# Optimization experiments

Measured on AMD Instinct MI355X. Metric: run time of the kernel, lower is better.

Reference implementation:

```python
import jax, jax.numpy as jnp
import numpy as np

N, E, B = 16000, 256000, 64
H = 4
DIMS = [960, 512, 256, 128]  # per-layer input dims; output dim of layer i is DIMS[i+1] = HID[i]*H
HID = [128, 64, 32]


def setup_inputs() -> dict:
    key = jax.random.key(0)
    ks = jax.random.split(key, 16)
    inp = {}
    inp["x"] = jax.random.normal(ks[0], (N, DIMS[0]), jnp.float32)
    inp["edge_index"] = jax.random.randint(ks[1], (2, E), 0, N)
    inp["batch"] = jnp.sort(jax.random.randint(ks[2], (N,), 0, B))
    k = 3
    for i in range(3):
        din, c = DIMS[i], HID[i]
        s = 1.0 / np.sqrt(din).astype(np.float32)
        inp[f"Wl{i+1}"] = jax.random.normal(ks[k], (din, H * c), jnp.float32) * s; k += 1
        inp[f"Wr{i+1}"] = jax.random.normal(ks[k], (din, H * c), jnp.float32) * s; k += 1
        inp[f"att{i+1}"] = jax.random.normal(ks[k], (H, c), jnp.float32) * (1.0 / np.sqrt(c).astype(np.float32)); k += 1
        inp[f"b{i+1}"] = jnp.zeros((H * c,), jnp.float32)
        inp[f"gnw{i+1}"] = jnp.ones((H * c,), jnp.float32)
        inp[f"gnb{i+1}"] = jnp.zeros((H * c,), jnp.float32)
        inp[f"gnm{i+1}"] = jnp.ones((H * c,), jnp.float32)
    d = DIMS[-1]
    inp["aW1"] = jax.random.normal(ks[k], (d, 128), jnp.float32) * (1.0 / np.sqrt(d).astype(np.float32)); k += 1
    inp["ab1"] = jnp.zeros((128,), jnp.float32)
    inp["aW2"] = jax.random.normal(ks[k], (128, 1), jnp.float32) * (1.0 / np.sqrt(128).astype(np.float32)); k += 1
    inp["ab2"] = jnp.zeros((1,), jnp.float32)
    return inp


def _gatv2(x, src, dst, Wl, Wr, att, bias):
    # PyG GATv2Conv, concat=True, negative_slope=0.2 (self-loops already in src/dst)
    n = x.shape[0]
    h, c = att.shape
    xl = (x @ Wl).reshape(n, h, c)
    xr = (x @ Wr).reshape(n, h, c)
    e = jax.nn.leaky_relu(xl[src] + xr[dst], negative_slope=0.2)  # [E,H,C]
    logit = jnp.einsum('ehc,hc->eh', e, att)                      # [E,H]
    m = jax.ops.segment_max(logit, dst, num_segments=n)
    m = jnp.nan_to_num(m, neginf=0.0)
    p = jnp.exp(logit - m[dst])
    z = jax.ops.segment_sum(p, dst, num_segments=n)
    alpha = p / (z[dst] + 1e-16)                                  # segment softmax over dst
    out = jax.ops.segment_sum(alpha[:, :, None] * xl[src], dst, num_segments=n)
    return out.reshape(n, h * c) + bias


def _graphnorm(x, w, b, ms, eps=1e-5):
    # PyG GraphNorm with batch=None: normalize over all nodes as one graph
    mean = jnp.mean(x, axis=0, keepdims=True)
    xc = x - ms * mean
    var = jnp.mean(xc * xc, axis=0, keepdims=True)
    return w * xc / jnp.sqrt(var + eps) + b


def reference(x, edge_index, batch,
              Wl1, Wr1, att1, b1, gnw1, gnb1, gnm1,
              Wl2, Wr2, att2, b2, gnw2, gnb2, gnm2,
              Wl3, Wr3, att3, b3, gnw3, gnb3, gnm3,
              aW1, ab1, aW2, ab2):
    n = x.shape[0]
    loop = jnp.arange(n)
    src = jnp.concatenate([edge_index[0], loop])  # add self-loops (PyG default)
    dst = jnp.concatenate([edge_index[1], loop])
    layers = [(Wl1, Wr1, att1, b1, gnw1, gnb1, gnm1),
              (Wl2, Wr2, att2, b2, gnw2, gnb2, gnm2),
              (Wl3, Wr3, att3, b3, gnw3, gnb3, gnm3)]
    for Wl, Wr, att, bb, gw, gb, gm in layers:
        x = _gatv2(x, src, dst, Wl, Wr, att, bb)
        x = _graphnorm(x, gw, gb, gm)
        x = jax.nn.relu(x)
    # AttentionalAggregation pooling: gate MLP -> segment softmax over graphs -> weighted sum
    gate = jax.nn.relu(x @ aW1 + ab1) @ aW2 + ab2  # [N,1]
    mg = jax.ops.segment_max(gate, batch, num_segments=B)
    mg = jnp.nan_to_num(mg, neginf=0.0)
    pg = jnp.exp(gate - mg[batch])
    zg = jax.ops.segment_sum(pg, batch, num_segments=B)
    a = pg / (zg[batch] + 1e-16)
    return jax.ops.segment_sum(a * x, batch, num_segments=B)  # [B, 128]
```

## Files before the change

### kernel.cpp

```cpp
#include <hip/hip_runtime.h>
#include <cstdint>
#include <cstddef>
#include <math.h>


typedef _Float16  h16x8  __attribute__((ext_vector_type(8)));
typedef _Float16  h16x4  __attribute__((ext_vector_type(4)));
typedef _Float16  h16x2  __attribute__((ext_vector_type(2)));
typedef float     f32x4  __attribute__((ext_vector_type(4)));

template<int R> struct HV;
template<> struct HV<8> { using T = h16x8; };
template<> struct HV<4> { using T = h16x4; };
template<> struct HV<2> { using T = h16x2; };

__device__ __forceinline__ void gload_lds16(const void* g, void* l) {
    __builtin_amdgcn_global_load_lds(
        (const __attribute__((address_space(1))) uint32_t*)g,
        (__attribute__((address_space(3))) uint32_t*)l, 16, 0, 0);
}

__device__ __forceinline__ int swz_k(int k, int row) {
    return (k & ~31) | ((((k >> 3) & 3) ^ ((row >> 1) & 3)) << 3) | (k & 7);
}

__device__ __forceinline__ void gn_coef(float s1, float s2, float w, float b,
                                        float ms, float invN, float& al, float& be) {
    float mean = s1 * invN;
    float ex2  = s2 * invN;
    float a    = ms * mean;
    float var  = ex2 - 2.f * a * mean + a * a;
    al = w * rsqrtf(var + 1e-5f);
    be = b - a * al;
}

__device__ __forceinline__ void conv_elem(int t, const float* __restrict__ Wl,
                                          const float* __restrict__ Wr,
                                          _Float16* __restrict__ Wt, int K, int HC) {
    int k = t / HC, n = t - k * HC;
    const int ks = swz_k(k, n);
    Wt[(size_t)n * K + ks] = (_Float16)Wl[t];
    if (Wr) Wt[(size_t)(HC + n) * K + ks] = (_Float16)Wr[t];
}

__global__ __launch_bounds__(256) void conv_all(
        const float* __restrict__ Wl0, const float* __restrict__ Wr0, _Float16* __restrict__ T0,
        const float* __restrict__ Wl1, const float* __restrict__ Wr1, _Float16* __restrict__ T1,
        const float* __restrict__ Wl2, const float* __restrict__ Wr2, _Float16* __restrict__ T2,
        const float* __restrict__ Wa, _Float16* __restrict__ Ta) {
    int t = blockIdx.x * blockDim.x + threadIdx.x;
    if (t < 491520) { conv_elem(t, Wl0, Wr0, T0, 960, 512); return; }
    t -= 491520;
    if (t < 131072) { conv_elem(t, Wl1, Wr1, T1, 512, 256); return; }
    t -= 131072;
    if (t < 32768)  { conv_elem(t, Wl2, Wr2, T2, 256, 128); return; }
    t -= 32768;
    if (t < 16384)  conv_elem(t, Wa, nullptr, Ta, 128, 128);
}

template<typename InT, bool NORM>
__global__ __launch_bounds__(256) void prep_a(
        const InT* __restrict__ X,
        const float* __restrict__ s1, const float* __restrict__ s2,
        const float* __restrict__ gw, const float* __restrict__ gb,
        const float* __restrict__ gm, float invN,
        _Float16* __restrict__ Out, int M, int K) {
    int t = blockIdx.x * blockDim.x + threadIdx.x;
    const int gpr = K >> 3;
    if (t >= M * gpr) return;
    int m = t / gpr, g = t - m * gpr;
    int k = g << 3;
    float uu[8];
    if constexpr (sizeof(InT) == 4) {
        const float* src = (const float*)X + (size_t)m * K + k;
        float4 u0 = *(const float4*)src;
        float4 u1 = *(const float4*)(src + 4);
        uu[0] = u0.x; uu[1] = u0.y; uu[2] = u0.z; uu[3] = u0.w;
        uu[4] = u1.x; uu[5] = u1.y; uu[6] = u1.z; uu[7] = u1.w;
    } else {
        h16x8 hv = *(const h16x8*)((const _Float16*)X + (size_t)m * K + k);
        #pragma unroll
        for (int j = 0; j < 8; ++j) uu[j] = (float)hv[j];
    }
    if (NORM) {
        #pragma unroll
        for (int j = 0; j < 8; ++j) {
            float al, be;
            gn_coef(s1[k + j], s2[k + j], gw[k + j], gb[k + j], gm[k + j],
                    invN, al, be);
            uu[j] = fmaxf(al * uu[j] + be, 0.f);
        }
    }
    h16x8 h;
    #pragma unroll
    for (int j = 0; j < 8; ++j) h[j] = (_Float16)uu[j];
    *(h16x8*)&Out[(size_t)m * K + swz_k(k, m)] = h;
}

template<bool BIAS, bool RELU, bool GATE, typename OutT>
__global__ __launch_bounds__(256) void mfma_gemm(
        const _Float16* __restrict__ A, const _Float16* __restrict__ Bt,
        const float* __restrict__ bias, OutT* __restrict__ C,
        OutT* __restrict__ C2, int CN,
        int M, int K, int N,
        const float* __restrict__ gw2, const float* __restrict__ gb2,
        float* __restrict__ gate) {
    __shared__ __attribute__((aligned(16))) _Float16 sA[2][128 * 32];
    __shared__ __attribute__((aligned(16))) _Float16 sB[2][128 * 32];
    __shared__ float gsum[128];

    const int gx  = gridDim.x;
    const int nwg = gx * gridDim.y;
    const int id  = blockIdx.y * gx + blockIdx.x;
    const int q   = nwg >> 3, r = nwg & 7;
    const int xcd = id & 7, sub = id >> 3;
    const int nid = (xcd < r) ? (xcd * (q + 1) + sub)
                              : (r * (q + 1) + (xcd - r) * q + sub);
    const int row0 = (nid / gx) * 128;
    const int col0 = (nid % gx) * 128;

    const int tid  = threadIdx.x;
    const int lane = tid & 63;
    const int w    = tid >> 6;
    const int wm   = w >> 1, wn = w & 1;
    const int lr   = lane & 15, lg = lane >> 4;
    const int bRow = w * 16 + (lane >> 2);
    const int bGrp = (lane & 3) * 8;
    const int fGrp = (lg ^ ((lr >> 1) & 3)) * 8;

    f32x4 acc[4][4] = {};

    const _Float16* pa = A  + (size_t)(row0 + bRow) * K + bGrp;
    const _Float16* pb = Bt + (size_t)(col0 + bRow) * K + bGrp;

    auto stage = [&](int buf, int k0) {
        gload_lds16(pa + k0,                  (char*)&sA[buf][0] + w * 1024);
        gload_lds16(pa + (size_t)64 * K + k0, (char*)&sA[buf][0] + 4096 + w * 1024);
        gload_lds16(pb + k0,                  (char*)&sB[buf][0] + w * 1024);
        gload_lds16(pb + (size_t)64 * K + k0, (char*)&sB[buf][0] + 4096 + w * 1024);
    };

    stage(0, 0);
    if (GATE) { if (tid < 128) gsum[tid] = 0.f; }
    __syncthreads();
    int cur = 0;
    for (int k0 = 0; k0 < K; k0 += 32) {
        if (k0 + 32 < K) stage(cur ^ 1, k0 + 32);
        h16x8 ah[4], bh[4];
        #pragma unroll
        for (int i = 0; i < 4; ++i) {
            ah[i] = *(const h16x8*)&sA[cur][(wm * 64 + i * 16 + lr) * 32 + fGrp];
            bh[i] = *(const h16x8*)&sB[cur][(wn * 64 + i * 16 + lr) * 32 + fGrp];
        }
        #pragma unroll
        for (int i = 0; i < 4; ++i)
            #pragma unroll
            for (int j = 0; j < 4; ++j)
                acc[i][j] = __builtin_amdgcn_mfma_f32_16x16x32_f16(ah[i], bh[j], acc[i][j], 0, 0, 0);
        __syncthreads();
        cur ^= 1;
    }

    if constexpr (!GATE) {
        OutT* co = (col0 < CN) ? C : C2;
        const int cb = (col0 < CN) ? col0 : col0 - CN;
        #pragma unroll
        for (int i = 0; i < 4; ++i) {
            const int rowb = row0 + wm * 64 + i * 16 + lg * 4;
            #pragma unroll
            for (int j = 0; j < 4; ++j) {
                const int col  = col0 + wn * 64 + j * 16 + lr;
                const int colw = cb   + wn * 64 + j * 16 + lr;
                const float bv = BIAS ? bias[col] : 0.f;
                #pragma unroll
                for (int qq = 0; qq < 4; ++qq) {
                    float v = acc[i][j][qq] + bv;
                    if (RELU) v = fmaxf(v, 0.f);
                    co[(size_t)(rowb + qq) * CN + colw] = (OutT)v;
                }
            }
        }
    } else {
        float gp[4][4] = {};
        float w2[4];
        #pragma unroll
        for (int j = 0; j < 4; ++j) w2[j] = gw2[wn * 64 + j * 16 + lr];
        #pragma unroll
        for (int i = 0; i < 4; ++i)
            #pragma unroll
            for (int j = 0; j < 4; ++j) {
                const int col = wn * 64 + j * 16 + lr;
                const float bv = bias[col];
                #pragma unroll
                for (int qq = 0; qq < 4; ++qq) {
                    float v = fmaxf(acc[i][j][qq] + bv, 0.f);
                    gp[i][qq] += v * w2[j];
                }
            }
        #pragma unroll
        for (int i = 0; i < 4; ++i)
            #pragma unroll
            for (int qq = 0; qq < 4; ++qq) {
                float pv = gp[i][qq];
                pv += __shfl_xor(pv, 1);
                pv += __shfl_xor(pv, 2);
                pv += __shfl_xor(pv, 4);
                pv += __shfl_xor(pv, 8);
                if (lr == 0) atomicAdd(&gsum[wm * 64 + i * 16 + lg * 4 + qq], pv);
            }
        __syncthreads();
        if (tid < 128) gate[row0 + tid] = gsum[tid] + gb2[0];
    }
}

__global__ void csr_count(const int* __restrict__ edst, int E, int Etot,
                          int* __restrict__ deg) {
    int e = blockIdx.x * blockDim.x + threadIdx.x;
    if (e >= Etot) return;
    int d = (e < E) ? edst[e] : e - E;
    atomicAdd(&deg[d], 1);
}

__global__ __launch_bounds__(1024) void scan_deg(const int* __restrict__ deg,
                                                 int* __restrict__ row_start,
                                                 int* __restrict__ cursor, int N) {
    __shared__ int part[1024];
    const int tid = threadIdx.x;
    const int base = tid * 16;
    int loc[16];
    int s = 0;
    #pragma unroll
    for (int j = 0; j < 16; ++j) {
        int i = base + j;
        s += (i < N) ? deg[i] : 0;
        loc[j] = s;
    }
    part[tid] = s; __syncthreads();
    #pragma unroll
    for (int off = 1; off < 1024; off <<= 1) {
        int t2 = (tid >= off) ? part[tid - off] : 0;
        __syncthreads();
        part[tid] += t2;
        __syncthreads();
    }
    const int pre = tid ? part[tid - 1] : 0;
    #pragma unroll
    for (int j = 0; j < 16; ++j) {
        int i = base + j;
        if (i < N) {
            int st = pre + (j ? loc[j - 1] : 0);
            row_start[i] = st;
            cursor[i]    = st;
            if (i == N - 1) row_start[N] = pre + loc[j];
        }
    }
}

__global__ void csr_fill(const int* __restrict__ esrc, const int* __restrict__ edst,
                         int E, int Etot, int* __restrict__ cursor,
                         int* __restrict__ src_perm) {
    int e = blockIdx.x * blockDim.x + threadIdx.x;
    if (e >= Etot) return;
    int s, d;
    if (e < E) { s = esrc[e]; d = edst[e]; }
    else       { s = d = e - E; }
    int pos = atomicAdd(&cursor[d], 1);
    src_perm[pos] = s;
}

template<int LOG2C>
__global__ __launch_bounds__(256) void gat_agg(
        const _Float16* __restrict__ xl, const _Float16* __restrict__ xr,
        const float* __restrict__ att, const float* __restrict__ bias,
        const int* __restrict__ row_start, const int* __restrict__ src_perm,
        int N, _Float16* __restrict__ out) {
    constexpr int HC  = 4 << LOG2C;
    constexpr int R   = HC / 64;
    constexpr int P   = R / 2;
    constexpr int U   = 8;
    using hvec = typename HV<R>::T;

    const int widx = threadIdx.x >> 6;
    const int lane = threadIdx.x & 63;
    const int dst  = blockIdx.x * 4 + widx;
    if (dst >= N) return;

    const int base = lane * R;
    h16x2 xr2[P], at2[P];
    float acc[R];
    {
        hvec xv = *(const hvec*)&xr[(size_t)dst * HC + base];
        const h16x2* xp = (const h16x2*)&xv;
        #pragma unroll
        for (int i = 0; i < P; ++i) {
            xr2[i] = xp[i];
            h16x2 t;
            t[0] = (_Float16)att[base + 2 * i];
            t[1] = (_Float16)att[base + 2 * i + 1];
            at2[i] = t;
        }
        #pragma unroll
        for (int it = 0; it < R; ++it) acc[it] = 0.f;
    }
    h16x2 zp; zp[0] = (_Float16)0.f;  zp[1] = (_Float16)0.f;
    h16x2 sl; sl[0] = (_Float16)0.2f; sl[1] = (_Float16)0.2f;

    float z = 0.f;
    const int start = row_start[dst], end = row_start[dst + 1];

    auto do_edge = [&](const hvec& row) {
        const h16x2* r2 = (const h16x2*)&row;
        float a = 0.f;
        #pragma unroll
        for (int i = 0; i < P; ++i) {
            h16x2 s  = r2[i] + xr2[i];
            h16x2 lk = __builtin_elementwise_max(s, zp)
                     + __builtin_elementwise_min(s, zp) * sl;
            a = __builtin_amdgcn_fdot2(lk, at2[i], a, false);
        }
        #pragma unroll
        for (int sh = 1; sh < 16; sh <<= 1) a += __shfl_xor(a, sh);
        float p = __expf(a);
        z += p;
        #pragma unroll
        for (int it = 0; it < R; ++it) acc[it] += p * (float)row[it];
    };

    int cs = start;
    for (; cs + U <= end; cs += U) {
        hvec rows[U];
        #pragma unroll
        for (int k = 0; k < U; ++k) {
            int src = __builtin_amdgcn_readfirstlane(src_perm[cs + k]);
            rows[k] = *(const hvec*)&xl[(size_t)src * HC + base];
        }
        #pragma unroll
        for (int k = 0; k < U; ++k) do_edge(rows[k]);
    }
    for (; cs < end; ++cs) {
        int src = __builtin_amdgcn_readfirstlane(src_perm[cs]);
        hvec row = *(const hvec*)&xl[(size_t)src * HC + base];
        do_edge(row);
    }

    const float inv = 1.f / (z + 1e-16f);
    hvec ov;
    #pragma unroll
    for (int it = 0; it < R; ++it)
        ov[it] = (_Float16)(acc[it] * inv + bias[base + it]);
    *(hvec*)&out[(size_t)dst * HC + base] = ov;
}

__global__ __launch_bounds__(64) void colstats(const _Float16* __restrict__ x, int HC,
                                               float* __restrict__ s1, float* __restrict__ s2) {
    int c  = blockIdx.x * 64 + threadIdx.x;
    int r0 = blockIdx.y * 128;
    float a = 0.f, b = 0.f;
    for (int r = r0; r < r0 + 128; ++r) {
        float v = (float)x[(size_t)r * HC + c];
        a += v; b += v * v;
    }
    atomicAdd(&s1[c], a);
    atomicAdd(&s2[c], b);
}

__global__ __launch_bounds__(1024) void attn_pool(
        const _Float16* __restrict__ x,
        const float* __restrict__ s1, const float* __restrict__ s2,
        const float* __restrict__ gw, const float* __restrict__ gb,
        const float* __restrict__ gm, float invN,
        const float* __restrict__ gate, const int* __restrict__ batch,
        int N, float* __restrict__ out) {
    const int b   = blockIdx.x;
    const int tid = threadIdx.x;
    const int grp = tid >> 7;
    const int ch  = tid & 127;
    int lo, hi;
    { int l = 0, r = N; while (l < r) { int mid = (l + r) >> 1; if (batch[mid] < b) l = mid + 1; else r = mid; } lo = l; }
    { int l = lo, r = N; while (l < r) { int mid = (l + r) >> 1; if (batch[mid] < b + 1) l = mid + 1; else r = mid; } hi = l; }
    if (lo >= hi) { if (tid < 128) out[b * 128 + tid] = 0.f; return; }

    float alc, bec;
    gn_coef(s1[ch], s2[ch], gw[ch], gb[ch], gm[ch], invN, alc, bec);

    __shared__ float red[1024];
    float mx = -INFINITY;
    for (int n = lo + tid; n < hi; n += 1024) mx = fmaxf(mx, gate[n]);
    red[tid] = mx; __syncthreads();
    for (int s = 512; s; s >>= 1) { if (tid < s) red[tid] = fmaxf(red[tid], red[tid + s]); __syncthreads(); }
    mx = red[0]; __syncthreads();
    float zs = 0.f;
    for (int n = lo + tid; n < hi; n += 1024) zs += __expf(gate[n] - mx);
    red[tid] = zs; __syncthreads();
    for (int s = 512; s; s >>= 1) { if (tid < s) red[tid] += red[tid + s]; __syncthreads(); }
    zs = red[0]; __syncthreads();
    float acc = 0.f;
    for (int n = lo + grp; n < hi; n += 8) {
        float wv = __expf(gate[n] - mx);
        float v  = fmaxf(alc * (float)x[(size_t)n * 128 + ch] + bec, 0.f);
        acc += wv * v;
    }
    red[tid] = acc; __syncthreads();
    if (tid < 128) {
        float s = red[tid];
        #pragma unroll
        for (int g = 1; g < 8; ++g) s += red[g * 128 + tid];
        out[b * 128 + tid] = s / (zs + 1e-16f);
    }
}

extern "C" void kernel_launch(void* const* d_in, const int* in_sizes, int n_in,
                              void* d_out, int out_size, void* d_ws, size_t ws_size,
                              hipStream_t stream) {
    const float* x0  = (const float*)d_in[0];
    const int* edge  = (const int*)d_in[1];
    const int* batch = (const int*)d_in[2];
    const int N = in_sizes[2];
    const int E = in_sizes[1] / 2;
    const int Etot = E + N;
    const int dims[4] = {960, 512, 256, 128};

    const float* Wl[3]   = {(const float*)d_in[3],  (const float*)d_in[10], (const float*)d_in[17]};
    const float* Wr[3]   = {(const float*)d_in[4],  (const float*)d_in[11], (const float*)d_in[18]};
    const float* attp[3] = {(const float*)d_in[5],  (const float*)d_in[12], (const float*)d_in[19]};
    const float* bi[3]   = {(const float*)d_in[6],  (const float*)d_in[13], (const float*)d_in[20]};
    const float* gw[3]   = {(const float*)d_in[7],  (const float*)d_in[14], (const float*)d_in[21]};
    const float* gb[3]   = {(const float*)d_in[8],  (const float*)d_in[15], (const float*)d_in[22]};
    const float* gm[3]   = {(const float*)d_in[9],  (const float*)d_in[16], (const float*)d_in[23]};
    const float* aW1 = (const float*)d_in[24];
    const float* ab1 = (const float*)d_in[25];
    const float* aW2 = (const float*)d_in[26];
    const float* ab2 = (const float*)d_in[27];

    size_t off = 0;
    auto alloc = [&](size_t bytes) -> char* {
        char* p = (char*)d_ws + off;
        off += (bytes + 255) & ~(size_t)255;
        return p;
    };
    _Float16* xlB     = (_Float16*)alloc((size_t)N * 512 * 2);
    _Float16* xrB     = (_Float16*)alloc((size_t)N * 512 * 2);
    _Float16* aT      = (_Float16*)alloc((size_t)N * 960 * 2);
    _Float16* bufC    = (_Float16*)alloc((size_t)N * 512 * 2);
    int*     deg      = (int*)alloc((size_t)N * 4);
    float*   s12      = (float*)alloc(3 * 1024 * 4);
    int*     row_start= (int*)alloc((size_t)(N + 1) * 4);
    int*     cursor   = (int*)alloc((size_t)N * 4);
    int*     src_perm = (int*)alloc((size_t)Etot * 4);
    float*   gateB    = (float*)alloc((size_t)N * 4);
    _Float16* wt[3];
    for (int l = 0; l < 3; ++l)
        wt[l] = (_Float16*)alloc((size_t)dims[l] * (2 * dims[l + 1]) * 2);
    _Float16* awt = (_Float16*)alloc(128 * 128 * 2);
    (void)ws_size; (void)n_in; (void)out_size;

    const float invN = 1.0f / N;

    conv_all<<<(671744 + 255) / 256, 256, 0, stream>>>(
        Wl[0], Wr[0], wt[0], Wl[1], Wr[1], wt[1], Wl[2], Wr[2], wt[2], aW1, awt);

    hipMemsetAsync(deg, 0, (size_t)N * 4 + 3 * 1024 * 4, stream);
    csr_count<<<(Etot + 255) / 256, 256, 0, stream>>>(edge + E, E, Etot, deg);
    scan_deg<<<1, 1024, 0, stream>>>(deg, row_start, cursor, N);
    csr_fill<<<(Etot + 255) / 256, 256, 0, stream>>>(edge, edge + E, E, Etot,
                                                     cursor, src_perm);

    for (int l = 0; l < 3; ++l) {
        const int K = dims[l], HC = dims[l + 1];
        const int ngrp = N * (K >> 3);
        if (l == 0)
            prep_a<float, false><<<(ngrp + 255) / 256, 256, 0, stream>>>(
                x0, nullptr, nullptr, nullptr, nullptr, nullptr, 0.f, aT, N, K);
        else
            prep_a<_Float16, true><<<(ngrp + 255) / 256, 256, 0, stream>>>(
                bufC, s12 + (l - 1) * 1024, s12 + (l - 1) * 1024 + 512,
                gw[l - 1], gb[l - 1], gm[l - 1], invN, aT, N, K);

        dim3 ggrid((2 * HC) / 128, N / 128);
        mfma_gemm<false, false, false, _Float16><<<ggrid, 256, 0, stream>>>(
            aT, wt[l], nullptr, xlB, xrB, HC, N, K, 2 * HC,
            nullptr, nullptr, nullptr);

        const int agrid = (N + 3) / 4;
        if (l == 0)      gat_agg<7><<<agrid, 256, 0, stream>>>(xlB, xrB, attp[l], bi[l], row_start, src_perm, N, bufC);
        else if (l == 1) gat_agg<6><<<agrid, 256, 0, stream>>>(xlB, xrB, attp[l], bi[l], row_start, src_perm, N, bufC);
        else             gat_agg<5><<<agrid, 256, 0, stream>>>(xlB, xrB, attp[l], bi[l], row_start, src_perm, N, bufC);

        colstats<<<dim3(HC / 64, N / 128), 64, 0, stream>>>(bufC, HC, s12 + l * 1024, s12 + l * 1024 + 512);
    }

    prep_a<_Float16, true><<<(N * 16 + 255) / 256, 256, 0, stream>>>(
        bufC, s12 + 2048, s12 + 2048 + 512, gw[2], gb[2], gm[2], invN, aT, N, 128);
    mfma_gemm<true, true, true, float><<<dim3(1, N / 128), 256, 0, stream>>>(
        aT, awt, ab1, nullptr, nullptr, 128, N, 128, 128, aW2, ab2, gateB);
    attn_pool<<<64, 1024, 0, stream>>>(bufC, s12 + 2048, s12 + 2048 + 512,
                                       gw[2], gb[2], gm[2], invN, gateB, batch, N, (float*)d_out);
}
```

Measured before the change: 320.2 us.

## Fuse A-operand conversion and GraphNorm+ReLU into GEMM prologue, drop prep_a

Removes the separate prep_a kernel that converted and normalized activations into a swizzled fp16 staging buffer. The GEMM now loads A directly from global memory into registers: fp32 input for layer 0, fp16 plus precomputed per-column GraphNorm coefficients held in LDS for later layers. It applies norm and ReLU, converts to fp16 and writes the swizzled tile into LDS, with the next tile's register loads overlapping the current MFMA work. This saves a full write and reread of the N×K A matrix and four kernel launches. In exchange, A no longer uses direct global-to-LDS loads, adds register pressure, and every column tile redundantly redoes the conversion and coefficient work.

```diff
diff --git a/kernel.cpp b/kernel.cpp
--- a/kernel.cpp
+++ b/kernel.cpp
@@ -58,56 +58,21 @@
     if (t < 16384)  conv_elem(t, Wa, nullptr, Ta, 128, 128);
 }
 
-template<typename InT, bool NORM>
-__global__ __launch_bounds__(256) void prep_a(
-        const InT* __restrict__ X,
-        const float* __restrict__ s1, const float* __restrict__ s2,
-        const float* __restrict__ gw, const float* __restrict__ gb,
-        const float* __restrict__ gm, float invN,
-        _Float16* __restrict__ Out, int M, int K) {
-    int t = blockIdx.x * blockDim.x + threadIdx.x;
-    const int gpr = K >> 3;
-    if (t >= M * gpr) return;
-    int m = t / gpr, g = t - m * gpr;
-    int k = g << 3;
-    float uu[8];
-    if constexpr (sizeof(InT) == 4) {
-        const float* src = (const float*)X + (size_t)m * K + k;
-        float4 u0 = *(const float4*)src;
-        float4 u1 = *(const float4*)(src + 4);
-        uu[0] = u0.x; uu[1] = u0.y; uu[2] = u0.z; uu[3] = u0.w;
-        uu[4] = u1.x; uu[5] = u1.y; uu[6] = u1.z; uu[7] = u1.w;
-    } else {
-        h16x8 hv = *(const h16x8*)((const _Float16*)X + (size_t)m * K + k);
-        #pragma unroll
-        for (int j = 0; j < 8; ++j) uu[j] = (float)hv[j];
-    }
-    if (NORM) {
-        #pragma unroll
-        for (int j = 0; j < 8; ++j) {
-            float al, be;
-            gn_coef(s1[k + j], s2[k + j], gw[k + j], gb[k + j], gm[k + j],
-                    invN, al, be);
-            uu[j] = fmaxf(al * uu[j] + be, 0.f);
-        }
-    }
-    h16x8 h;
-    #pragma unroll
-    for (int j = 0; j < 8; ++j) h[j] = (_Float16)uu[j];
-    *(h16x8*)&Out[(size_t)m * K + swz_k(k, m)] = h;
-}
-
-template<bool BIAS, bool RELU, bool GATE, typename OutT>
+template<int AMODE, bool BIAS, bool RELU, bool GATE, typename OutT>
 __global__ __launch_bounds__(256) void mfma_gemm(
-        const _Float16* __restrict__ A, const _Float16* __restrict__ Bt,
+        const void* __restrict__ Ap, const _Float16* __restrict__ Bt,
         const float* __restrict__ bias, OutT* __restrict__ C,
         OutT* __restrict__ C2, int CN,
         int M, int K, int N,
+        const float* __restrict__ ns1, const float* __restrict__ ns2,
+        const float* __restrict__ ngw, const float* __restrict__ ngb,
+        const float* __restrict__ ngm, float invN,
         const float* __restrict__ gw2, const float* __restrict__ gb2,
         float* __restrict__ gate) {
     __shared__ __attribute__((aligned(16))) _Float16 sA[2][128 * 32];
     __shared__ __attribute__((aligned(16))) _Float16 sB[2][128 * 32];
-    __shared__ float gsum[128];
+    __shared__ float2 cof[(AMODE == 1) ? 960 : 1];
+    __shared__ float gsum[GATE ? 128 : 1];
 
     const int gx  = gridDim.x;
     const int nwg = gx * gridDim.y;
@@ -124,28 +89,85 @@
     const int w    = tid >> 6;
     const int wm   = w >> 1, wn = w & 1;
     const int lr   = lane & 15, lg = lane >> 4;
+    const int sr   = tid >> 2;
+    const int sg   = tid & 3;
     const int bRow = w * 16 + (lane >> 2);
     const int bGrp = (lane & 3) * 8;
     const int fGrp = (lg ^ ((lr >> 1) & 3)) * 8;
 
     f32x4 acc[4][4] = {};
 
-    const _Float16* pa = A  + (size_t)(row0 + bRow) * K + bGrp;
-    const _Float16* pb = Bt + (size_t)(col0 + bRow) * K + bGrp;
-
-    auto stage = [&](int buf, int k0) {
-        gload_lds16(pa + k0,                  (char*)&sA[buf][0] + w * 1024);
-        gload_lds16(pa + (size_t)64 * K + k0, (char*)&sA[buf][0] + 4096 + w * 1024);
+    const _Float16* pa16 = (const _Float16*)Ap + (size_t)(row0 + sr) * K + sg * 8;
+    const float*    pa32 = (const float*)Ap    + (size_t)(row0 + sr) * K + sg * 8;
+    const _Float16* pb   = Bt + (size_t)(col0 + bRow) * K + bGrp;
+
+    h16x8 ar16[2];
+    f32x4 ar32[4];
+
+    auto a_load = [&](int k0) {
+        if constexpr (AMODE == 1) {
+            ar16[0] = *(const h16x8*)(pa16 + k0);
+            ar16[1] = *(const h16x8*)(pa16 + (size_t)64 * K + k0);
+        } else {
+            ar32[0] = *(const f32x4*)(pa32 + k0);
+            ar32[1] = *(const f32x4*)(pa32 + k0 + 4);
+            ar32[2] = *(const f32x4*)(pa32 + (size_t)64 * K + k0);
+            ar32[3] = *(const f32x4*)(pa32 + (size_t)64 * K + k0 + 4);
+        }
+    };
+    auto a_write = [&](int buf, int k0) {
+        float alv[8], bev[8];
+        if constexpr (AMODE == 1) {
+            #pragma unroll
+            for (int j = 0; j < 8; ++j) {
+                float2 cv = cof[k0 + sg * 8 + j];
+                alv[j] = cv.x;
+                bev[j] = cv.y;
+            }
+        }
+        #pragma unroll
+        for (int h = 0; h < 2; ++h) {
+            const int rr = sr + h * 64;
+            float uu[8];
+            if constexpr (AMODE == 1) {
+                #pragma unroll
+                for (int j = 0; j < 8; ++j)
+                    uu[j] = fmaxf(alv[j] * (float)ar16[h][j] + bev[j], 0.f);
+            } else {
+                uu[0] = ar32[2*h][0]; uu[1] = ar32[2*h][1];
+                uu[2] = ar32[2*h][2]; uu[3] = ar32[2*h][3];
+                uu[4] = ar32[2*h+1][0]; uu[5] = ar32[2*h+1][1];
+                uu[6] = ar32[2*h+1][2]; uu[7] = ar32[2*h+1][3];
+            }
+            h16x8 hv;
+            #pragma unroll
+            for (int j = 0; j < 8; ++j) hv[j] = (_Float16)uu[j];
+            *(h16x8*)&sA[buf][rr * 32 + ((sg ^ ((rr >> 1) & 3)) << 3)] = hv;
+        }
+    };
+    auto b_stage = [&](int buf, int k0) {
         gload_lds16(pb + k0,                  (char*)&sB[buf][0] + w * 1024);
         gload_lds16(pb + (size_t)64 * K + k0, (char*)&sB[buf][0] + 4096 + w * 1024);
     };
 
-    stage(0, 0);
+    if constexpr (AMODE == 1) {
+        for (int c = tid; c < K; c += 256) {
+            float al_, be_;
+            gn_coef(ns1[c], ns2[c], ngw[c], ngb[c], ngm[c], invN, al_, be_);
+            cof[c] = make_float2(al_, be_);
+        }
+    }
     if (GATE) { if (tid < 128) gsum[tid] = 0.f; }
+    a_load(0);
+    b_stage(0, 0);
     __syncthreads();
+    a_write(0, 0);
+    __syncthreads();
+
     int cur = 0;
     for (int k0 = 0; k0 < K; k0 += 32) {
-        if (k0 + 32 < K) stage(cur ^ 1, k0 + 32);
+        const bool more = (k0 + 32 < K);
+        if (more) { a_load(k0 + 32); b_stage(cur ^ 1, k0 + 32); }
         h16x8 ah[4], bh[4];
         #pragma unroll
         for (int i = 0; i < 4; ++i) {
@@ -157,6 +179,7 @@
             #pragma unroll
             for (int j = 0; j < 4; ++j)
                 acc[i][j] = __builtin_amdgcn_mfma_f32_16x16x32_f16(ah[i], bh[j], acc[i][j], 0, 0, 0);
+        if (more) a_write(cur ^ 1, k0 + 32);
         __syncthreads();
         cur ^= 1;
     }
@@ -440,7 +463,6 @@
     };
     _Float16* xlB     = (_Float16*)alloc((size_t)N * 512 * 2);
     _Float16* xrB     = (_Float16*)alloc((size_t)N * 512 * 2);
-    _Float16* aT      = (_Float16*)alloc((size_t)N * 960 * 2);
     _Float16* bufC    = (_Float16*)alloc((size_t)N * 512 * 2);
     int*     deg      = (int*)alloc((size_t)N * 4);
     float*   s12      = (float*)alloc(3 * 1024 * 4);
@@ -467,19 +489,18 @@
 
     for (int l = 0; l < 3; ++l) {
         const int K = dims[l], HC = dims[l + 1];
-        const int ngrp = N * (K >> 3);
+        dim3 ggrid((2 * HC) / 128, N / 128);
         if (l == 0)
-            prep_a<float, false><<<(ngrp + 255) / 256, 256, 0, stream>>>(
-                x0, nullptr, nullptr, nullptr, nullptr, nullptr, 0.f, aT, N, K);
+            mfma_gemm<2, false, false, false, _Float16><<<ggrid, 256, 0, stream>>>(
+                x0, wt[0], nullptr, xlB, xrB, HC, N, K, 2 * HC,
+                nullptr, nullptr, nullptr, nullptr, nullptr, 0.f,
+                nullptr, nullptr, nullptr);
         else
-            prep_a<_Float16, true><<<(ngrp + 255) / 256, 256, 0, stream>>>(
-                bufC, s12 + (l - 1) * 1024, s12 + (l - 1) * 1024 + 512,
-                gw[l - 1], gb[l - 1], gm[l - 1], invN, aT, N, K);
-
-        dim3 ggrid((2 * HC) / 128, N / 128);
-        mfma_gemm<false, false, false, _Float16><<<ggrid, 256, 0, stream>>>(
-            aT, wt[l], nullptr, xlB, xrB, HC, N, K, 2 * HC,
-            nullptr, nullptr, nullptr);
+            mfma_gemm<1, false, false, false, _Float16><<<ggrid, 256, 0, stream>>>(
+                bufC, wt[l], nullptr, xlB, xrB, HC, N, K, 2 * HC,
+                s12 + (l - 1) * 1024, s12 + (l - 1) * 1024 + 512,
+                gw[l - 1], gb[l - 1], gm[l - 1], invN,
+                nullptr, nullptr, nullptr);
 
         const int agrid = (N + 3) / 4;
         if (l == 0)      gat_agg<7><<<agrid, 256, 0, stream>>>(xlB, xrB, attp[l], bi[l], row_start, src_perm, N, bufC);
@@ -489,10 +510,10 @@
         colstats<<<dim3(HC / 64, N / 128), 64, 0, stream>>>(bufC, HC, s12 + l * 1024, s12 + l * 1024 + 512);
     }
 
-    prep_a<_Float16, true><<<(N * 16 + 255) / 256, 256, 0, stream>>>(
-        bufC, s12 + 2048, s12 + 2048 + 512, gw[2], gb[2], gm[2], invN, aT, N, 128);
-    mfma_gemm<true, true, true, float><<<dim3(1, N / 128), 256, 0, stream>>>(
-        aT, awt, ab1, nullptr, nullptr, 128, N, 128, 128, aW2, ab2, gateB);
+    mfma_gemm<1, true, true, true, float><<<dim3(1, N / 128), 256, 0, stream>>>(
+        bufC, awt, ab1, nullptr, nullptr, 128, N, 128, 128,
+        s12 + 2048, s12 + 2048 + 512, gw[2], gb[2], gm[2], invN,
+        aW2, ab2, gateB);
     attn_pool<<<64, 1024, 0, stream>>>(bufC, s12 + 2048, s12 + 2048 + 512,
                                        gw[2], gb[2], gm[2], invN, gateB, batch, N, (float*)d_out);
 }
```

Result: faster. 304.2 us (-5.0%).
